# Kernel tuning notes

Hardware: AMD Instinct MI355X
Metric: run time of the kernel (lower is better)

The kernel has to match this reference:

```python
import jax, jax.numpy as jnp
import numpy as np

TEMP = 0.07
EPS = 1e-6
NORM_EPS = 1e-12  # F.normalize default eps
LN_EPS = 1e-5

B, D, H, W = 32, 256, 64, 64
K = 256
DFF = 2048


def _l2norm(v, axis):
    n = jnp.sqrt(jnp.sum(v * v, axis=axis, keepdims=True))
    return v / jnp.maximum(n, NORM_EPS)


def _layernorm(v, g, b):
    mu = jnp.mean(v, axis=-1, keepdims=True)
    var = jnp.mean((v - mu) ** 2, axis=-1, keepdims=True)
    return (v - mu) * jax.lax.rsqrt(var + LN_EPS) * g + b


def setup_inputs() -> dict:
    key = jax.random.key(0)
    ks = jax.random.split(key, 8)
    s1 = 1.0 / np.sqrt(D)
    s2 = 1.0 / np.sqrt(DFF)
    return {
        "x": jax.random.normal(ks[0], (B, D, H, W), jnp.float32),
        "tgt": jax.random.normal(ks[1], (B, K, D), jnp.float32),
        "w1": jax.random.uniform(ks[2], (DFF, D), jnp.float32, -s1, s1),
        "b1": jax.random.uniform(ks[3], (DFF,), jnp.float32, -s1, s1),
        "w2": jax.random.uniform(ks[4], (D, DFF), jnp.float32, -s2, s2),
        "b2": jax.random.uniform(ks[5], (D,), jnp.float32, -s2, s2),
        "g2": jnp.ones((D,), jnp.float32),
        "be2": jnp.zeros((D,), jnp.float32),
        "g3": jnp.ones((D,), jnp.float32),
        "be3": jnp.zeros((D,), jnp.float32),
    }


def reference(x, tgt, w1, b1, w2, b2, g2, be2, g3, be3):
    # slot cross-attention with L2-normalized q/k
    tn = _l2norm(tgt, axis=2)           # (b,k,d)
    xn = _l2norm(x, axis=1)             # (b,d,h,w)
    dots = jnp.einsum('bkd,bdhw->bkhw', tn, xn)
    attn = jax.nn.softmax(dots / TEMP, axis=1) + EPS          # softmax over slots
    attn = attn / jnp.sum(attn, axis=(2, 3), keepdims=True)   # spatial normalization
    tgt2 = jnp.einsum('bdhw,bkhw->bkd', x, attn)
    t = _layernorm(tgt + tgt2, g2, be2)
    # FFN (dropout = identity in eval)
    ff = jnp.maximum(t @ w1.T + b1, 0.0) @ w2.T + b2
    return _layernorm(t + ff, g3, be3)
```

## Files before the change

### kernel.cpp

```cpp
#include <hip/hip_runtime.h>
#include <hip/hip_bf16.h>

using bf16 = __hip_bfloat16;

typedef __attribute__((ext_vector_type(8))) short short8;
typedef __attribute__((ext_vector_type(4))) float f32x4;

constexpr int Bb = 32, Dd = 256, HWw = 4096, Kk = 256, Ff = 2048;
constexpr float TEMP_INV = 1.0f / 0.07f;
constexpr float EPSf = 1e-6f;
constexpr float NORM_EPSf = 1e-12f;
constexpr float LN_EPSf = 1e-5f;

static __device__ __forceinline__ float b2f(bf16 v) { return __bfloat162float(v); }
static __device__ __forceinline__ bf16 f2b(float v) { return __float2bfloat16(v); }


__global__ __launch_bounds__(64) void k_tn(const float* __restrict__ tgt,
                                           bf16* __restrict__ tnbf) {
  int row = blockIdx.x;
  int b = row >> 8, slot = row & 255;
  int lane = threadIdx.x;
  const float* src = tgt + (size_t)row * Dd + lane * 4;
  float v[4];
#pragma unroll
  for (int u = 0; u < 4; u++) v[u] = src[u];
  float ss = v[0] * v[0] + v[1] * v[1] + v[2] * v[2] + v[3] * v[3];
#pragma unroll
  for (int m = 32; m >= 1; m >>= 1) ss += __shfl_xor(ss, m, 64);
  float inv = 1.0f / fmaxf(sqrtf(ss), NORM_EPSf);
  bf16 o[4] __attribute__((aligned(8)));
#pragma unroll
  for (int u = 0; u < 4; u++) o[u] = f2b(v[u] * inv);
  int s = lane >> 3;
  int q2 = (lane >> 1) & 3;
  int jh = (lane & 1) * 4;
  size_t fi = (size_t)((slot >> 4) * 64 + q2 * 16 + (slot & 15));
  *(float2*)(tnbf + ((size_t)(b * 8 + s) * 1024 + fi) * 8 + jh) = *(float2*)o;
}

__global__ __launch_bounds__(64) void k_prew1(const float* __restrict__ w1,
                                              bf16* __restrict__ w1bf) {
  int f = blockIdx.x;
  int lane = threadIdx.x;
  const float* src = w1 + (size_t)f * Dd + lane * 4;
  bf16 o[4] __attribute__((aligned(8)));
#pragma unroll
  for (int u = 0; u < 4; u++) o[u] = f2b(src[u]);
  int s = lane >> 3;
  int q2 = (lane >> 1) & 3;
  int jh = (lane & 1) * 4;
  size_t fi = (size_t)(((f & 63) >> 4) * 64 + q2 * 16 + (f & 15));
  *(float2*)(w1bf + ((size_t)((f >> 6) * 8 + s) * 256 + fi) * 8 + jh) = *(float2*)o;
}

__global__ __launch_bounds__(64) void k_prew2(const float* __restrict__ w2,
                                              bf16* __restrict__ w2bf) {
  int d = blockIdx.x;
  int lane = threadIdx.x;
  const float* src = w2 + (size_t)d * Ff + lane * 32;
  size_t gbase = (size_t)((d >> 6) * 64 + lane) * 256;
  int fbase = ((d & 63) >> 4) * 64 + (d & 15);
#pragma unroll
  for (int q2 = 0; q2 < 4; q2++) {
    float4 v0 = *(const float4*)(src + q2 * 8);
    float4 v1 = *(const float4*)(src + q2 * 8 + 4);
    bf16 o[8] __attribute__((aligned(16)));
    o[0] = f2b(v0.x); o[1] = f2b(v0.y); o[2] = f2b(v0.z); o[3] = f2b(v0.w);
    o[4] = f2b(v1.x); o[5] = f2b(v1.y); o[6] = f2b(v1.z); o[7] = f2b(v1.w);
    *(float4*)(w2bf + (gbase + fbase + q2 * 16) * 8) = *(float4*)o;
  }
}

#define MFMA16(a, b, c) __builtin_amdgcn_mfma_f32_16x16x32_bf16(a, b, c, 0, 0, 0)

__global__ __launch_bounds__(256) void k_dots(const bf16* __restrict__ tnbf,
                                              const float* __restrict__ x,
                                              bf16* __restrict__ xb_bf,
                                              bf16* __restrict__ attn_bf,
                                              float* __restrict__ S) {
  __shared__ __align__(16) char smem[16384];
  bf16* Bs = (bf16*)smem;
  float* ssred = (float*)(smem + 8320);
  float* nxl = (float*)(smem + 12672);
  float* red = (float*)(smem + 12928);
  int b = blockIdx.x >> 6;
  int hw0 = (blockIdx.x & 63) * 64;
  int tid = threadIdx.x;
  int wave = tid >> 6, lane = tid & 63;
  int quad = lane >> 4, nl = lane & 15;

  int dp = tid >> 4;
  int ch = tid & 15;
  int qb = dp >> 2;
  int jb = (dp & 3) * 2;

  f32x4 acc[4][4];
#pragma unroll
  for (int i = 0; i < 4; i++)
#pragma unroll
    for (int j = 0; j < 4; j++) acc[i][j] = (f32x4){0.f, 0.f, 0.f, 0.f};
  float ssp[4] = {0.f, 0.f, 0.f, 0.f};

  int spx = (hw0 >> 5) + (ch >> 3);
  int q2x = (ch >> 1) & 3;
  int jx = (ch & 1) * 4;

  float4 va, vb;
  short8 afp[4];
  {
    const float* xr0 = x + (size_t)((b << 8) + 2 * dp) * HWw + hw0 + ch * 4;
    va = *(const float4*)xr0;
    vb = *(const float4*)(xr0 + HWw);
    const bf16* ts0 = tnbf + (size_t)(b * 8) * 1024 * 8;
#pragma unroll
    for (int mt = 0; mt < 4; mt++)
      afp[mt] = *(const short8*)(ts0 + (size_t)(((wave << 2) + mt) * 64 + lane) * 8);
  }

  for (int s = 0; s < 8; s++) {
    bf16* bsb = Bs + (s & 1) * 2080;
    bf16 pa[4] __attribute__((aligned(8)));
    bf16 pb[4] __attribute__((aligned(8)));
    {
      float vva[4] = {va.x, va.y, va.z, va.w};
      float vvb[4] = {vb.x, vb.y, vb.z, vb.w};
#pragma unroll
      for (int jj = 0; jj < 4; jj++) {
        ssp[jj] += vva[jj] * vva[jj] + vvb[jj] * vvb[jj];
        pa[jj] = f2b(vva[jj]);
        pb[jj] = f2b(vvb[jj]);
      }
#pragma unroll
      for (int jj = 0; jj < 4; jj++) {
        int hwl = ch * 4 + jj;
        int nt = hwl >> 4;
        int li = (qb << 4) | (hwl & 15);
        union { bf16 h[2]; unsigned int u; } pk;
        pk.h[0] = pa[jj];
        pk.h[1] = pb[jj];
        *(unsigned int*)&bsb[nt * 520 + li * 8 + jb] = pk.u;
      }
    }
    short8 af[4];
#pragma unroll
    for (int mt = 0; mt < 4; mt++) af[mt] = afp[mt];
    __syncthreads();
    {
      int d0r = s * 32 + 2 * dp;
      int fiA = (d0r >> 4) * 64 + q2x * 16 + (d0r & 15);
      size_t base = ((size_t)(b * 128) + spx) * 1024;
      *(float2*)(xb_bf + (base + fiA) * 8 + jx) = *(float2*)pa;
      *(float2*)(xb_bf + (base + fiA + 1) * 8 + jx) = *(float2*)pb;
    }
    if (s < 7) {
      const float* xr = x + (size_t)((b << 8) + (s + 1) * 32 + 2 * dp) * HWw + hw0 + ch * 4;
      va = *(const float4*)xr;
      vb = *(const float4*)(xr + HWw);
      const bf16* tsrc = tnbf + (size_t)(b * 8 + s + 1) * 1024 * 8;
#pragma unroll
      for (int mt = 0; mt < 4; mt++)
        afp[mt] = *(const short8*)(tsrc + (size_t)(((wave << 2) + mt) * 64 + lane) * 8);
    }
    short8 bfv[4];
#pragma unroll
    for (int nt = 0; nt < 4; nt++)
      bfv[nt] = *(const short8*)(bsb + nt * 520 + lane * 8);
#pragma unroll
    for (int mt = 0; mt < 4; mt++)
#pragma unroll
      for (int nt = 0; nt < 4; nt++) acc[mt][nt] = MFMA16(af[mt], bfv[nt], acc[mt][nt]);
  }

#pragma unroll
  for (int jj = 0; jj < 4; jj++) ssred[(ch * 4 + jj) * 17 + dp] = ssp[jj];
  __syncthreads();
  if (tid < 64) {
    float sum = 0.f;
#pragma unroll
    for (int i = 0; i < 16; i++) sum += ssred[tid * 17 + i];
    nxl[tid] = TEMP_INV / fmaxf(sqrtf(sum), NORM_EPSf);
  }
  __syncthreads();

  float sc[4];
#pragma unroll
  for (int nt = 0; nt < 4; nt++) sc[nt] = nxl[nt * 16 + nl];
#pragma unroll
  for (int mt = 0; mt < 4; mt++)
#pragma unroll
    for (int nt = 0; nt < 4; nt++)
#pragma unroll
      for (int r = 0; r < 4; r++) acc[mt][nt][r] *= sc[nt];

  float* red2 = red + 256;

  float pmax[4];
#pragma unroll
  for (int nt = 0; nt < 4; nt++) {
    float m = acc[0][nt][0];
#pragma unroll
    for (int mt = 0; mt < 4; mt++)
#pragma unroll
      for (int r = 0; r < 4; r++) m = fmaxf(m, acc[mt][nt][r]);
    m = fmaxf(m, __shfl_xor(m, 16, 64));
    m = fmaxf(m, __shfl_xor(m, 32, 64));
    pmax[nt] = m;
  }
  if (lane < 16) {
#pragma unroll
    for (int nt = 0; nt < 4; nt++) red[((wave << 2) + nt) * 16 + nl] = pmax[nt];
  }
  __syncthreads();
  float cmax[4];
#pragma unroll
  for (int nt = 0; nt < 4; nt++) {
    float m = red[nt * 16 + nl];
#pragma unroll
    for (int w2 = 1; w2 < 4; w2++) m = fmaxf(m, red[((w2 << 2) + nt) * 16 + nl]);
    cmax[nt] = m;
  }

  float psum[4];
#pragma unroll
  for (int nt = 0; nt < 4; nt++) {
    float s = 0.f;
#pragma unroll
    for (int mt = 0; mt < 4; mt++)
#pragma unroll
      for (int r = 0; r < 4; r++) {
        float e = __expf(acc[mt][nt][r] - cmax[nt]);
        acc[mt][nt][r] = e;
        s += e;
      }
    s += __shfl_xor(s, 16, 64);
    s += __shfl_xor(s, 32, 64);
    psum[nt] = s;
  }
  if (lane < 16) {
#pragma unroll
    for (int nt = 0; nt < 4; nt++) red2[((wave << 2) + nt) * 16 + nl] = psum[nt];
  }
  __syncthreads();
  float ci[4];
#pragma unroll
  for (int nt = 0; nt < 4; nt++) {
    float s = 0.f;
#pragma unroll
    for (int w2 = 0; w2 < 4; w2++) s += red2[((w2 << 2) + nt) * 16 + nl];
    ci[nt] = 1.0f / s;
  }

#pragma unroll
  for (int mt = 0; mt < 4; mt++) {
    int slotg = (b << 8) + (wave << 6) + (mt << 4) + (quad << 2);
#pragma unroll
    for (int r = 0; r < 4; r++) {
      float rs = 0.f;
#pragma unroll
      for (int nt = 0; nt < 4; nt++) {
        bf16 hb = f2b(acc[mt][nt][r] * ci[nt] + EPSf);
        float q = b2f(hb);
        acc[mt][nt][r] = q;
        rs += q;
      }
      rs += __shfl_xor(rs, 1, 64);
      rs += __shfl_xor(rs, 2, 64);
      rs += __shfl_xor(rs, 4, 64);
      rs += __shfl_xor(rs, 8, 64);
      if (nl == 0) atomicAdd(&S[slotg + r], rs);
    }
  }

  __syncthreads();
  bf16* rp = (bf16*)smem;
  int jat = nl & 7;
#pragma unroll
  for (int h = 0; h < 2; h++) {
#pragma unroll
    for (int mt = 0; mt < 4; mt++) {
      int fi0 = ((wave << 2) + mt) * 64 + (quad << 2);
#pragma unroll
      for (int ntl = 0; ntl < 2; ntl++) {
        int nt = (h << 1) + ntl;
        int q2p = (ntl << 1) + (nl >> 3);
#pragma unroll
        for (int r = 0; r < 4; r++) {
          int fi = fi0 + q2p * 16 + r;
          int fisw = fi ^ ((fi >> 3) & 3);
          rp[fisw * 8 + jat] = f2b(acc[mt][nt][r]);
        }
      }
    }
    __syncthreads();
    size_t gbase = ((size_t)(b * 128) + (hw0 >> 5) + h) * 1024 * 8;
#pragma unroll
    for (int u = 0; u < 4; u++) {
      int fl = u * 256 + tid;
      int fg = fl ^ ((fl >> 3) & 3);
      short8 vv = *(const short8*)(rp + (size_t)fl * 8);
      *(short8*)(attn_bf + gbase + (size_t)fg * 8) = vv;
    }
    if (h == 0) __syncthreads();
  }
}

__global__ __launch_bounds__(256) void k_gemm2(const bf16* __restrict__ attn_bf,
                                               const bf16* __restrict__ xb_bf,
                                               float* __restrict__ t2) {
  int n = blockIdx.x;
  int b = n & 31;
  int r2 = n >> 5;
  int kp = r2 & 3;
  int dgrp = r2 >> 2;
  int tid = threadIdx.x;
  int wave = tid >> 6, lane = tid & 63;
  int wr = wave >> 1, wc = wave & 1;

  f32x4 acc[2][2];
#pragma unroll
  for (int i = 0; i < 2; i++)
#pragma unroll
    for (int j = 0; j < 2; j++) acc[i][j] = (f32x4){0.f, 0.f, 0.f, 0.f};

  const bf16* Abase = attn_bf + ((size_t)(b * 128) * 1024 + (size_t)(kp * 4 + wr * 2) * 64) * 8;
  const bf16* Bbase = xb_bf + ((size_t)(b * 128) * 1024 + (size_t)(dgrp * 4 + wc * 2) * 64) * 8;
#pragma unroll 4
  for (int st = 0; st < 128; st++) {
    const bf16* Ap = Abase + (size_t)st * 1024 * 8;
    const bf16* Bp = Bbase + (size_t)st * 1024 * 8;
    short8 a0 = *(const short8*)(Ap + (size_t)lane * 8);
    short8 a1 = *(const short8*)(Ap + (size_t)(64 + lane) * 8);
    short8 b0 = *(const short8*)(Bp + (size_t)lane * 8);
    short8 b1 = *(const short8*)(Bp + (size_t)(64 + lane) * 8);
    acc[0][0] = MFMA16(a0, b0, acc[0][0]);
    acc[0][1] = MFMA16(a0, b1, acc[0][1]);
    acc[1][0] = MFMA16(a1, b0, acc[1][0]);
    acc[1][1] = MFMA16(a1, b1, acc[1][1]);
  }
  int quad = lane >> 4, nl = lane & 15;
#pragma unroll
  for (int i = 0; i < 2; i++)
#pragma unroll
    for (int r = 0; r < 4; r++) {
      int row = (b << 8) + kp * 64 + wr * 32 + i * 16 + quad * 4 + r;
#pragma unroll
      for (int j = 0; j < 2; j++) {
        int col = dgrp * 64 + wc * 32 + j * 16 + nl;
        t2[(size_t)row * Dd + col] = acc[i][j][r];
      }
    }
}

__global__ __launch_bounds__(64) void k_ln_pre(const float* __restrict__ t2,
                                               const float* __restrict__ S,
                                               const float* __restrict__ tgt,
                                               const float* __restrict__ g,
                                               const float* __restrict__ be,
                                               float* __restrict__ t,
                                               bf16* __restrict__ tbf) {
  int row = blockIdx.x;
  int lane = threadIdx.x;
  float sInv = 1.0f / S[row];
  size_t off = (size_t)row * Dd + lane * 4;
  float4 a0 = *(const float4*)(t2 + off);
  const float* pt = tgt + off;
  float v[4];
  v[0] = a0.x * sInv + pt[0];
  v[1] = a0.y * sInv + pt[1];
  v[2] = a0.z * sInv + pt[2];
  v[3] = a0.w * sInv + pt[3];
  float s1 = v[0] + v[1] + v[2] + v[3];
  float s2 = v[0] * v[0] + v[1] * v[1] + v[2] * v[2] + v[3] * v[3];
#pragma unroll
  for (int m = 32; m >= 1; m >>= 1) {
    s1 += __shfl_xor(s1, m, 64);
    s2 += __shfl_xor(s2, m, 64);
  }
  float mu = s1 * (1.0f / 256.0f);
  float var = s2 * (1.0f / 256.0f) - mu * mu;
  float rs = rsqrtf(fmaxf(var, 0.f) + LN_EPSf);
  float* po = t + (size_t)row * Dd + lane * 4;
  bf16 o[4] __attribute__((aligned(8)));
#pragma unroll
  for (int u = 0; u < 4; u++) {
    float val = (v[u] - mu) * rs * g[lane * 4 + u] + be[lane * 4 + u];
    po[u] = val;
    o[u] = f2b(val);
  }
  int s = lane >> 3;
  int q2 = (lane >> 1) & 3;
  int jh = (lane & 1) * 4;
  size_t fi = (size_t)(((row & 63) >> 4) * 64 + q2 * 16 + (row & 15));
  *(float2*)(tbf + ((size_t)((row >> 6) * 8 + s) * 256 + fi) * 8 + jh) = *(float2*)o;
}

__global__ __launch_bounds__(256) void k_ffn1(const bf16* __restrict__ tbf,
                                              const bf16* __restrict__ w1bf,
                                              const float* __restrict__ b1,
                                              bf16* __restrict__ h1bf) {
  __shared__ __align__(16) bf16 rp[512 * 8];
  int rowgrp = blockIdx.x >> 5;
  int fgrp = blockIdx.x & 31;
  int tid = threadIdx.x;
  int wave = tid >> 6, lane = tid & 63;
  int am = (wave >> 1) * 2, bn = (wave & 1) * 2;

  f32x4 acc[2][2];
#pragma unroll
  for (int i = 0; i < 2; i++)
#pragma unroll
    for (int j = 0; j < 2; j++) acc[i][j] = (f32x4){0.f, 0.f, 0.f, 0.f};

  const bf16* Abase = tbf + (size_t)rowgrp * 8 * 256 * 8;
  const bf16* Bbase = w1bf + (size_t)fgrp * 8 * 256 * 8;
#pragma unroll
  for (int s = 0; s < 8; s++) {
    short8 af[2], bfr[2];
#pragma unroll
    for (int i = 0; i < 2; i++)
      af[i] = *(const short8*)(Abase + ((size_t)s * 256 + ((am + i) * 64 + lane)) * 8);
#pragma unroll
    for (int j = 0; j < 2; j++)
      bfr[j] = *(const short8*)(Bbase + ((size_t)s * 256 + ((bn + j) * 64 + lane)) * 8);
#pragma unroll
    for (int i = 0; i < 2; i++)
#pragma unroll
      for (int j = 0; j < 2; j++) acc[i][j] = MFMA16(af[i], bfr[j], acc[i][j]);
  }
  int quad = lane >> 4, nl = lane & 15;
  int jat = nl & 7;
#pragma unroll
  for (int j = 0; j < 2; j++) {
    int f = fgrp * 64 + (bn + j) * 16 + nl;
    float bias = b1[f];
    int seth = (bn + j) >> 1;
    int q2p = ((bn + j) & 1) * 2 + (nl >> 3);
#pragma unroll
    for (int i = 0; i < 2; i++) {
      int fiBase = (am + i) * 64 + q2p * 16 + (quad << 2);
#pragma unroll
      for (int r = 0; r < 4; r++) {
        float val = fmaxf(acc[i][j][r] + bias, 0.f);
        int fi = fiBase + r;
        int fisw = fi ^ ((fi >> 3) & 3);
        rp[(seth * 256 + fisw) * 8 + jat] = f2b(val);
      }
    }
  }
  __syncthreads();
  size_t sp0 = (size_t)(rowgrp * 64) + fgrp * 2;
#pragma unroll
  for (int u = 0; u < 2; u++) {
    int loc = tid;
    int fg = loc ^ ((loc >> 3) & 3);
    short8 vv = *(const short8*)(rp + ((size_t)u * 256 + loc) * 8);
    *(short8*)(h1bf + ((sp0 + u) * 256 + fg) * 8) = vv;
  }
}

__global__ __launch_bounds__(256) void k_ffn2(const bf16* __restrict__ h1bf,
                                              const bf16* __restrict__ w2bf,
                                              float* __restrict__ o2) {
  __shared__ float redsm[4 * 4160];
  int n = blockIdx.x;
  int rowgrp = n >> 2;
  int cg = n & 3;
  int tid = threadIdx.x;
  int wave = tid >> 6, lane = tid & 63;

  f32x4 acc[4][4];
#pragma unroll
  for (int i = 0; i < 4; i++)
#pragma unroll
    for (int j = 0; j < 4; j++) acc[i][j] = (f32x4){0.f, 0.f, 0.f, 0.f};

#pragma unroll 4
  for (int stl = 0; stl < 16; stl++) {
    int sg = wave * 16 + stl;
    const bf16* Ab = h1bf + ((size_t)(rowgrp * 64 + sg) * 256) * 8;
    const bf16* Bbv = w2bf + ((size_t)(cg * 64 + sg) * 256) * 8;
    short8 af[4], bfr[4];
#pragma unroll
    for (int mt = 0; mt < 4; mt++)
      af[mt] = *(const short8*)(Ab + (size_t)(mt * 64 + lane) * 8);
#pragma unroll
    for (int nt = 0; nt < 4; nt++)
      bfr[nt] = *(const short8*)(Bbv + (size_t)(nt * 64 + lane) * 8);
#pragma unroll
    for (int mt = 0; mt < 4; mt++)
#pragma unroll
      for (int nt = 0; nt < 4; nt++) acc[mt][nt] = MFMA16(af[mt], bfr[nt], acc[mt][nt]);
  }
  int quad = lane >> 4, nl = lane & 15;
  float* my = redsm + wave * 4160;
#pragma unroll
  for (int mt = 0; mt < 4; mt++)
#pragma unroll
    for (int r = 0; r < 4; r++) {
      int row = mt * 16 + quad * 4 + r;
#pragma unroll
      for (int nt = 0; nt < 4; nt++)
        my[row * 65 + nt * 16 + nl] = acc[mt][nt][r];
    }
  __syncthreads();
#pragma unroll
  for (int u = 0; u < 16; u++) {
    int o = u * 256 + tid;
    int row = o >> 6, col = o & 63;
    int li = row * 65 + col;
    float ssum = redsm[li] + redsm[4160 + li] + redsm[8320 + li] + redsm[12480 + li];
    o2[(size_t)(rowgrp * 64 + row) * Dd + cg * 64 + col] = ssum;
  }
}

__global__ __launch_bounds__(64) void k_ln_out(const float* __restrict__ o2,
                                               const float* __restrict__ b2v,
                                               const float* __restrict__ t,
                                               const float* __restrict__ g,
                                               const float* __restrict__ be,
                                               float* __restrict__ out) {
  int row = blockIdx.x;
  int lane = threadIdx.x;
  size_t off = (size_t)row * Dd + lane * 4;
  float4 aq = *(const float4*)(o2 + off);
  const float* pt = t + off;
  float v[4];
  v[0] = aq.x + b2v[lane * 4 + 0] + pt[0];
  v[1] = aq.y + b2v[lane * 4 + 1] + pt[1];
  v[2] = aq.z + b2v[lane * 4 + 2] + pt[2];
  v[3] = aq.w + b2v[lane * 4 + 3] + pt[3];
  float s1 = v[0] + v[1] + v[2] + v[3];
  float s2 = v[0] * v[0] + v[1] * v[1] + v[2] * v[2] + v[3] * v[3];
#pragma unroll
  for (int m = 32; m >= 1; m >>= 1) {
    s1 += __shfl_xor(s1, m, 64);
    s2 += __shfl_xor(s2, m, 64);
  }
  float mu = s1 * (1.0f / 256.0f);
  float var = s2 * (1.0f / 256.0f) - mu * mu;
  float rs = rsqrtf(fmaxf(var, 0.f) + LN_EPSf);
  float* pw = out + (size_t)row * Dd + lane * 4;
#pragma unroll
  for (int u = 0; u < 4; u++)
    pw[u] = (v[u] - mu) * rs * g[lane * 4 + u] + be[lane * 4 + u];
}

extern "C" void kernel_launch(void* const* d_in, const int* in_sizes, int n_in,
                              void* d_out, int out_size, void* d_ws, size_t ws_size,
                              hipStream_t stream) {
  const float* x = (const float*)d_in[0];
  const float* tgt = (const float*)d_in[1];
  const float* w1 = (const float*)d_in[2];
  const float* b1 = (const float*)d_in[3];
  const float* w2 = (const float*)d_in[4];
  const float* b2v = (const float*)d_in[5];
  const float* g2 = (const float*)d_in[6];
  const float* be2 = (const float*)d_in[7];
  const float* g3 = (const float*)d_in[8];
  const float* be3 = (const float*)d_in[9];
  float* out = (float*)d_out;

  char* w = (char*)d_ws;
  bf16* tnbf = (bf16*)w;     w += (size_t)Bb * Kk * Dd * 2;
  float* S = (float*)w;      w += (size_t)Bb * Kk * 4;
  float* t = (float*)w;      w += (size_t)Bb * Kk * Dd * 4;
  bf16* attn_bf = (bf16*)w;  w += (size_t)Bb * HWw * Kk * 2;
  bf16* h1bf = (bf16*)w;     w += (size_t)Bb * Kk * Ff * 2;
  bf16* xb_bf = (bf16*)w;    w += (size_t)Bb * Dd * HWw * 2;

  bf16* tbf = tnbf;
  bf16* w1bf = attn_bf;
  bf16* w2bf = attn_bf + (size_t)Ff * Dd;
  float* t2 = (float*)h1bf;
  float* o2 = (float*)xb_bf;

  hipMemsetAsync(S, 0, (size_t)Bb * Kk * 4, stream);
  k_tn<<<Bb * Kk, 64, 0, stream>>>(tgt, tnbf);
  k_dots<<<Bb * (HWw / 64), 256, 0, stream>>>(tnbf, x, xb_bf, attn_bf, S);
  k_gemm2<<<512, 256, 0, stream>>>(attn_bf, xb_bf, t2);
  k_prew1<<<Ff, 64, 0, stream>>>(w1, w1bf);
  k_prew2<<<Dd, 64, 0, stream>>>(w2, w2bf);
  k_ln_pre<<<Bb * Kk, 64, 0, stream>>>(t2, S, tgt, g2, be2, t, tbf);
  k_ffn1<<<(Bb * Kk / 64) * (Ff / 64), 256, 0, stream>>>(tbf, w1bf, b1, h1bf);
  k_ffn2<<<512, 256, 0, stream>>>(h1bf, w2bf, o2);
  k_ln_out<<<Bb * Kk, 64, 0, stream>>>(o2, b2v, t, g3, be3, out);
}
```

Measured before the change: 407.7 us.

## Stage full x tile into LDS upfront, removing per-step barriers in dots loop

The k_dots kernel used to convert and stage one 32-channel slice of x per iteration into a double-buffered LDS tile, with a barrier before each step's MFMAs. It now loads all eight slices in two batches of four wide global loads, writes them all to a larger LDS buffer, synchronizes once, then runs the MFMA loop with no barriers. This raises memory-level parallelism and removes seven barriers. In exchange it grows shared memory from 16 KB to about 39 KB per block, which can lower occupancy, and it loses overlap between the x loads and the MFMA work.

```diff
diff --git a/kernel.cpp b/kernel.cpp
--- a/kernel.cpp
+++ b/kernel.cpp
@@ -79,11 +79,11 @@
                                               bf16* __restrict__ xb_bf,
                                               bf16* __restrict__ attn_bf,
                                               float* __restrict__ S) {
-  __shared__ __align__(16) char smem[16384];
-  bf16* Bs = (bf16*)smem;
-  float* ssred = (float*)(smem + 8320);
-  float* nxl = (float*)(smem + 12672);
-  float* red = (float*)(smem + 12928);
+  __shared__ __align__(16) char smem[39936];
+  bf16* Bs8 = (bf16*)smem;
+  float* ssred = (float*)(smem + 33280);
+  float* nxl = (float*)(smem + 37632);
+  float* red = (float*)(smem + 37888);
   int b = blockIdx.x >> 6;
   int hw0 = (blockIdx.x & 63) * 64;
   int tid = threadIdx.x;
@@ -106,31 +106,33 @@
   int q2x = (ch >> 1) & 3;
   int jx = (ch & 1) * 4;
 
-  float4 va, vb;
-  short8 afp[4];
-  {
-    const float* xr0 = x + (size_t)((b << 8) + 2 * dp) * HWw + hw0 + ch * 4;
-    va = *(const float4*)xr0;
-    vb = *(const float4*)(xr0 + HWw);
-    const bf16* ts0 = tnbf + (size_t)(b * 8) * 1024 * 8;
-#pragma unroll
-    for (int mt = 0; mt < 4; mt++)
-      afp[mt] = *(const short8*)(ts0 + (size_t)(((wave << 2) + mt) * 64 + lane) * 8);
-  }
-
-  for (int s = 0; s < 8; s++) {
-    bf16* bsb = Bs + (s & 1) * 2080;
-    bf16 pa[4] __attribute__((aligned(8)));
-    bf16 pb[4] __attribute__((aligned(8)));
-    {
-      float vva[4] = {va.x, va.y, va.z, va.w};
-      float vvb[4] = {vb.x, vb.y, vb.z, vb.w};
+#pragma unroll 1
+  for (int c = 0; c < 2; c++) {
+    float4 va4[4], vb4[4];
+#pragma unroll
+    for (int q = 0; q < 4; q++) {
+      const float* xr = x + (size_t)((b << 8) + (c * 4 + q) * 32 + 2 * dp) * HWw + hw0 + ch * 4;
+      va4[q] = *(const float4*)xr;
+      vb4[q] = *(const float4*)(xr + HWw);
+    }
+#pragma unroll
+    for (int q = 0; q < 4; q++) {
+      int s = c * 4 + q;
+      float vva[4] = {va4[q].x, va4[q].y, va4[q].z, va4[q].w};
+      float vvb[4] = {vb4[q].x, vb4[q].y, vb4[q].z, vb4[q].w};
+      bf16 pa[4] __attribute__((aligned(8)));
+      bf16 pb[4] __attribute__((aligned(8)));
 #pragma unroll
       for (int jj = 0; jj < 4; jj++) {
         ssp[jj] += vva[jj] * vva[jj] + vvb[jj] * vvb[jj];
         pa[jj] = f2b(vva[jj]);
         pb[jj] = f2b(vvb[jj]);
       }
+      int d0r = s * 32 + 2 * dp;
+      int fiA = (d0r >> 4) * 64 + q2x * 16 + (d0r & 15);
+      size_t base = ((size_t)(b * 128) + spx) * 1024;
+      *(float2*)(xb_bf + (base + fiA) * 8 + jx) = *(float2*)pa;
+      *(float2*)(xb_bf + (base + fiA + 1) * 8 + jx) = *(float2*)pb;
 #pragma unroll
       for (int jj = 0; jj < 4; jj++) {
         int hwl = ch * 4 + jj;
@@ -139,24 +141,24 @@
         union { bf16 h[2]; unsigned int u; } pk;
         pk.h[0] = pa[jj];
         pk.h[1] = pb[jj];
-        *(unsigned int*)&bsb[nt * 520 + li * 8 + jb] = pk.u;
-      }
-    }
+        *(unsigned int*)&Bs8[s * 2080 + nt * 520 + li * 8 + jb] = pk.u;
+      }
+    }
+  }
+  __syncthreads();
+
+  short8 afp[4];
+  {
+    const bf16* ts0 = tnbf + (size_t)(b * 8) * 1024 * 8;
+#pragma unroll
+    for (int mt = 0; mt < 4; mt++)
+      afp[mt] = *(const short8*)(ts0 + (size_t)(((wave << 2) + mt) * 64 + lane) * 8);
+  }
+  for (int s = 0; s < 8; s++) {
     short8 af[4];
 #pragma unroll
     for (int mt = 0; mt < 4; mt++) af[mt] = afp[mt];
-    __syncthreads();
-    {
-      int d0r = s * 32 + 2 * dp;
-      int fiA = (d0r >> 4) * 64 + q2x * 16 + (d0r & 15);
-      size_t base = ((size_t)(b * 128) + spx) * 1024;
-      *(float2*)(xb_bf + (base + fiA) * 8 + jx) = *(float2*)pa;
-      *(float2*)(xb_bf + (base + fiA + 1) * 8 + jx) = *(float2*)pb;
-    }
     if (s < 7) {
-      const float* xr = x + (size_t)((b << 8) + (s + 1) * 32 + 2 * dp) * HWw + hw0 + ch * 4;
-      va = *(const float4*)xr;
-      vb = *(const float4*)(xr + HWw);
       const bf16* tsrc = tnbf + (size_t)(b * 8 + s + 1) * 1024 * 8;
 #pragma unroll
       for (int mt = 0; mt < 4; mt++)
@@ -165,7 +167,7 @@
     short8 bfv[4];
 #pragma unroll
     for (int nt = 0; nt < 4; nt++)
-      bfv[nt] = *(const short8*)(bsb + nt * 520 + lane * 8);
+      bfv[nt] = *(const short8*)(Bs8 + s * 2080 + nt * 520 + lane * 8);
 #pragma unroll
     for (int mt = 0; mt < 4; mt++)
 #pragma unroll
```

After: 425.6 us. 4.4% more time.
